# Performance work log

Hardware: AMD Instinct MI355X
Metric: run time of the kernel (lower is better)

Reference implementation:

```python
import jax, jax.numpy as jnp
import numpy as np

H = 2048

def setup_inputs() -> dict:
    key = jax.random.key(0)
    ks = jax.random.split(key, 7)
    s = 1.0 / np.sqrt(H)
    return {
        "input": jax.random.normal(ks[0], (2, 4096, H), dtype=jnp.float32),
        "Wq": jax.random.uniform(ks[1], (H, H), jnp.float32, -s, s),
        "bq": jax.random.uniform(ks[2], (H,), jnp.float32, -s, s),
        "Wk": jax.random.uniform(ks[3], (H, H), jnp.float32, -s, s),
        "bk": jax.random.uniform(ks[4], (H,), jnp.float32, -s, s),
        "Wv": jax.random.uniform(ks[5], (H, H), jnp.float32, -s, s),
        "bv": jax.random.uniform(ks[6], (H,), jnp.float32, -s, s),
    }

def reference(input, Wq, bq, Wk, bk, Wv, bv):
    # Linear projections: y = x @ W^T + b (torch nn.Linear convention)
    q = jnp.einsum('bsh,oh->bso', input, Wq) + bq
    k = jnp.einsum('bsh,oh->bso', input, Wk) + bk
    v = jnp.einsum('bsh,oh->bso', input, Wv) + bv
    # NOTE: original module has NO 1/sqrt(d) scaling and NO mask
    scores = jnp.einsum('bqh,bkh->bqk', q, k)          # [B,S,S]
    attn = jax.nn.softmax(scores, axis=-1)
    out = jnp.einsum('bqk,bkh->bqh', attn, v)           # [B,S,H]
    return out
```

## Files before the change

kernel.cpp:

```cpp
#include <hip/hip_runtime.h>
#include <hip/hip_bf16.h>
#include <cstdint>
#include <cstddef>


typedef _Float16 half8 __attribute__((ext_vector_type(8)));
typedef _Float16 half4 __attribute__((ext_vector_type(4)));
typedef float    f32x4 __attribute__((ext_vector_type(4)));

__device__ __forceinline__ void gld_lds16(const void* g, void* l) {
  __builtin_amdgcn_global_load_lds(
      (const __attribute__((address_space(1))) unsigned int*)g,
      (__attribute__((address_space(3))) unsigned int*)l, 16, 0, 0);
}

#define FENCE()  asm volatile("" ::: "memory")
#define VMC(n)   asm volatile("s_waitcnt vmcnt(" #n ")" ::: "memory")
#define SBARF()  do { __builtin_amdgcn_s_barrier(); FENCE(); } while (0)
#define PRIO1()  __builtin_amdgcn_s_setprio(1)
#define PRIO0()  __builtin_amdgcn_s_setprio(0)

#define LOAD_A(dst, RB, MH) do {                                            \
  const char* _p = ldsA + ((RB)*2 + wr) * 16384 + fr * 128;                 \
  _Pragma("unroll") for (int mi = 0; mi < 4; ++mi) {                        \
    dst[mi][0] = *(const half8*)(_p + ((MH)*4 + mi) * 2048 + cS0);          \
    dst[mi][1] = *(const half8*)(_p + ((MH)*4 + mi) * 2048 + cS1);          \
  }                                                                         \
} while (0)

#define LOAD_B(dst, RB, NH) do {                                            \
  const char* _p = ldsB + ((RB)*2 + (wc >> 1)) * 16384 +                    \
                   ((wc & 1) * 64 + fr) * 128;                              \
  _Pragma("unroll") for (int ni = 0; ni < 2; ++ni) {                        \
    dst[ni][0] = *(const half8*)(_p + ((NH)*2 + ni) * 2048 + cS0);          \
    dst[ni][1] = *(const half8*)(_p + ((NH)*2 + ni) * 2048 + cS1);          \
  }                                                                         \
} while (0)

#define MFMA_Q(AF, BF, MH, NH)                                              \
  _Pragma("unroll") for (int mi = 0; mi < 4; ++mi)                          \
  _Pragma("unroll") for (int ni = 0; ni < 2; ++ni) {                        \
    f32x4& _c = acc[(MH)*4 + mi][(NH)*2 + ni];                              \
    _c = __builtin_amdgcn_mfma_f32_16x16x32_f16(AF[mi][0], BF[ni][0], _c, 0, 0, 0); \
    _c = __builtin_amdgcn_mfma_f32_16x16x32_f16(AF[mi][1], BF[ni][1], _c, 0, 0, 0); \
  }

#define STAGE8(BSEL, KO) do {                                               \
  const size_t _k = (KO);                                                   \
  gld_lds16(Asrc + _k,               ldsc + (BSEL)*32768 + wvd);            \
  gld_lds16(Asrc + _k + lda8,        ldsc + (BSEL)*32768 + wvd + 1024);     \
  gld_lds16(Asrc + _k + ldaH,        ldsc + (BSEL)*32768 + 16384 + wvd);    \
  gld_lds16(Asrc + _k + ldaH + lda8, ldsc + (BSEL)*32768 + 16384 + wvd + 1024); \
  gld_lds16(Bsrc + _k,               ldsc + 65536 + (BSEL)*32768 + wvd);    \
  gld_lds16(Bsrc + _k + ldb8,        ldsc + 65536 + (BSEL)*32768 + wvd + 1024); \
  gld_lds16(Bsrc + _k + ldbH,        ldsc + 65536 + (BSEL)*32768 + 16384 + wvd); \
  gld_lds16(Bsrc + _k + ldbH + ldb8, ldsc + 65536 + (BSEL)*32768 + 16384 + wvd + 1024); \
} while (0)

#define TILEB(RB, KO, DO_STAGE) do {                                        \
  LOAD_A(af0, RB, 0);                                                       \
  LOAD_B(b0,  RB, 0);                                                       \
  if (DO_STAGE) STAGE8((RB)^1, KO);                                         \
  LOAD_B(b1,  RB, 1);                                                       \
  LOAD_A(af1, RB, 1);                                                       \
  PRIO1();                                                                  \
  MFMA_Q(af0, b0, 0, 0);                                                    \
  MFMA_Q(af0, b1, 0, 1);                                                    \
  MFMA_Q(af1, b1, 1, 1);                                                    \
  MFMA_Q(af1, b0, 1, 0);                                                    \
  PRIO0();                                                                  \
  VMC(0);                                                                   \
  SBARF();                                                                  \
} while (0)

template <int MODE>
__global__ __launch_bounds__(512, 2) void gemm256(
    const _Float16* __restrict__ A, int lda,
    const _Float16* __restrict__ B, int ldb,
    const float* __restrict__ bias,
    void* __restrict__ out, int ldo, int K,
    size_t sA, size_t sB, size_t sO)
{
  __shared__ __attribute__((aligned(128))) char lds[131072];
  char* ldsc = (char*)lds;
  char* ldsA = ldsc;
  char* ldsB = ldsc + 65536;

  const int tid  = threadIdx.x;
  const int wv   = tid >> 6;
  const int lane = tid & 63;
  const int wr = wv >> 2;
  const int wc = wv & 3;
  const int bm = blockIdx.x * 256;
  const int bn = blockIdx.y * 256;
  A += (size_t)blockIdx.z * sA;
  B += (size_t)blockIdx.z * sB;

  const int fr = lane & 15;
  const int kq = lane >> 4;
  const int sx = (fr & 7) << 4;
  const int cS0 = (kq * 16) ^ sx;
  const int cS1 = (64 + kq * 16) ^ sx;
  const int lr  = lane >> 3;
  const int sc8 = ((lane & 7) ^ (lr & 7)) << 3;

  const _Float16* Asrc = A + (size_t)(bm + wv * 16 + lr) * lda + sc8;
  const _Float16* Bsrc = B + (size_t)(bn + wv * 16 + lr) * ldb + sc8;
  const size_t lda8 = (size_t)lda * 8,  ldaH = (size_t)lda * 128;
  const size_t ldb8 = (size_t)ldb * 8,  ldbH = (size_t)ldb * 128;
  const int wvd = wv * 2048;

  f32x4 acc[8][4];
  const f32x4 zf = {0.f, 0.f, 0.f, 0.f};
#pragma unroll
  for (int mi = 0; mi < 8; ++mi)
#pragma unroll
    for (int ni = 0; ni < 4; ++ni) acc[mi][ni] = zf;

  half8 af0[4][2], af1[4][2], b0[2][2], b1[2][2];

  const int NT = K >> 6;
  const int NI = NT >> 1;

  STAGE8(0, 0);
  VMC(0);
  SBARF();

  for (int it = 0; it < NI; ++it) {
    const size_t kA = (size_t)(2 * it + 1) * 64;
    const size_t kB = (size_t)(2 * it + 2) * 64;
    const bool sB = (2 * it + 2) < NT;
    TILEB(0, kA, 1);
    TILEB(1, kB, sB);
  }

#pragma unroll
  for (int mi = 0; mi < 8; ++mi) {
#pragma unroll
    for (int ni = 0; ni < 4; ++ni) {
      const int col  = bn + wc * 64 + ni * 16 + fr;
      const int row0 = bm + wr * 128 + mi * 16 + kq * 4;
      const f32x4 a = acc[mi][ni];
      if constexpr (MODE == 0) {
        float* O = (float*)out + (size_t)blockIdx.z * sO;
#pragma unroll
        for (int j = 0; j < 4; ++j) O[(size_t)(row0 + j) * ldo + col] = a[j];
      } else if constexpr (MODE == 1) {
        _Float16* O = (_Float16*)out;
        const float bb = bias[col];
#pragma unroll
        for (int j = 0; j < 4; ++j)
          O[(size_t)(row0 + j) * ldo + col] = (_Float16)(a[j] + bb);
      } else {
        _Float16* O = (_Float16*)out;
        const float bb = bias[col];
        half4 h;
#pragma unroll
        for (int j = 0; j < 4; ++j) h[j] = (_Float16)(a[j] + bb);
        *(half4*)(O + (size_t)col * ldo + row0) = h;
      }
    }
  }
}

__device__ __forceinline__ float wave_max_f(float v) {
#pragma unroll
  for (int o = 32; o; o >>= 1) v = fmaxf(v, __shfl_xor(v, o));
  return v;
}
__device__ __forceinline__ float wave_sum_f(float v) {
#pragma unroll
  for (int o = 32; o; o >>= 1) v += __shfl_xor(v, o);
  return v;
}

__global__ __launch_bounds__(256) void softmax_rows(
    const float* __restrict__ S, _Float16* __restrict__ P)
{
  __shared__ float rmax[4], rsum[4];
  const int tid = threadIdx.x;
  const float* s = S + (size_t)blockIdx.x * 4096;
  _Float16*    p = P + (size_t)blockIdx.x * 4096;

  f32x4 v[4];
  float m = -3.0e38f;
#pragma unroll
  for (int i = 0; i < 4; ++i) {
    v[i] = ((const f32x4*)s)[i * 256 + tid];
#pragma unroll
    for (int j = 0; j < 4; ++j) m = fmaxf(m, v[i][j]);
  }
  m = wave_max_f(m);
  if ((tid & 63) == 0) rmax[tid >> 6] = m;
  __syncthreads();
  m = fmaxf(fmaxf(rmax[0], rmax[1]), fmaxf(rmax[2], rmax[3]));

  float e[16];
  float sum = 0.f;
#pragma unroll
  for (int i = 0; i < 4; ++i)
#pragma unroll
    for (int j = 0; j < 4; ++j) {
      const float t = __expf(v[i][j] - m);
      e[i * 4 + j] = t;
      sum += t;
    }
  sum = wave_sum_f(sum);
  if ((tid & 63) == 0) rsum[tid >> 6] = sum;
  __syncthreads();
  sum = rsum[0] + rsum[1] + rsum[2] + rsum[3];
  const float inv = 1.0f / sum;

#pragma unroll
  for (int i = 0; i < 4; ++i) {
    half4 h;
#pragma unroll
    for (int j = 0; j < 4; ++j) h[j] = (_Float16)(e[i * 4 + j] * inv);
    ((half4*)p)[i * 256 + tid] = h;
  }
}

__global__ __launch_bounds__(256) void cvt_f32_f16(
    const float* __restrict__ in, _Float16* __restrict__ out, int n4)
{
  const int stride = gridDim.x * 256;
  for (int idx = blockIdx.x * 256 + threadIdx.x; idx < n4; idx += stride) {
    const f32x4 x = ((const f32x4*)in)[idx];
    half4 h;
#pragma unroll
    for (int j = 0; j < 4; ++j) h[j] = (_Float16)x[j];
    ((half4*)out)[idx] = h;
  }
}

extern "C" void kernel_launch(void* const* d_in, const int* in_sizes, int n_in,
                              void* d_out, int out_size, void* d_ws, size_t ws_size,
                              hipStream_t stream)
{
  const float* X  = (const float*)d_in[0];
  const float* Wq = (const float*)d_in[1];
  const float* bq = (const float*)d_in[2];
  const float* Wk = (const float*)d_in[3];
  const float* bk = (const float*)d_in[4];
  const float* Wv = (const float*)d_in[5];
  const float* bv = (const float*)d_in[6];
  float* out = (float*)d_out;

  const size_t NX = (size_t)2 * 4096 * 2048;
  const size_t NW = (size_t)2048 * 2048;
  const size_t NS = (size_t)2 * 4096 * 4096;

  char* w = (char*)d_ws;
  float*    Ssc = (float*)w;
  _Float16* Xh  = (_Float16*)w;
  _Float16* Wqh = (_Float16*)(w + NX * 2);
  _Float16* Wkh = (_Float16*)(w + NX * 2 + NW * 2);
  _Float16* Wvh = (_Float16*)(w + NX * 2 + 2 * NW * 2);
  _Float16* Q   = (_Float16*)(w + NS * 4);
  _Float16* Kp  = (_Float16*)(w + NS * 4 + NX * 2);
  _Float16* P   = (_Float16*)(w + NS * 4);
  _Float16* Vt  = (_Float16*)(w + NS * 4 + 2 * NX * 2);

  cvt_f32_f16<<<2048, 256, 0, stream>>>(X,  Xh,  (int)(NX / 4));
  cvt_f32_f16<<<512,  256, 0, stream>>>(Wq, Wqh, (int)(NW / 4));
  cvt_f32_f16<<<512,  256, 0, stream>>>(Wk, Wkh, (int)(NW / 4));
  cvt_f32_f16<<<512,  256, 0, stream>>>(Wv, Wvh, (int)(NW / 4));

  const dim3 blk(512);
  gemm256<1><<<dim3(32, 8, 1), blk, 0, stream>>>(Xh, 2048, Wqh, 2048, bq,
                                                 Q, 2048, 2048, 0, 0, 0);
  gemm256<1><<<dim3(32, 8, 1), blk, 0, stream>>>(Xh, 2048, Wkh, 2048, bk,
                                                 Kp, 2048, 2048, 0, 0, 0);
  gemm256<2><<<dim3(32, 8, 1), blk, 0, stream>>>(Xh, 2048, Wvh, 2048, bv,
                                                 Vt, 8192, 2048, 0, 0, 0);
  gemm256<0><<<dim3(16, 16, 2), blk, 0, stream>>>(
      Q, 2048, Kp, 2048, nullptr, Ssc, 4096, 2048,
      (size_t)4096 * 2048, (size_t)4096 * 2048, (size_t)4096 * 4096);
  softmax_rows<<<8192, 256, 0, stream>>>(Ssc, P);
  gemm256<0><<<dim3(16, 8, 2), blk, 0, stream>>>(
      P, 4096, Vt, 8192, nullptr, out, 2048, 4096,
      (size_t)4096 * 4096, (size_t)4096, (size_t)4096 * 2048);
}
```

Measured before the change: 548.4 us.

## Restructure GEMM main loop into eight-phase ping-pong schedule with split staging

Replaces the two-tile-per-iteration GEMM loop with an eight-phase schedule. Each phase interleaves one LDS fragment read, one half of a global-to-LDS stage, and one MFMA quadrant, separated by barriers and lgkm/vm waits. B tiles are prefetched further ahead and wait counts are relaxed so global loads can overlap several compute phases. It also drops the min-blocks-per-CU launch bound, which frees register allocation at possible occupancy cost, and reuses one A fragment buffer to cut registers. The extra barriers and waits add synchronisation overhead.

```diff
diff --git a/kernel.cpp b/kernel.cpp
--- a/kernel.cpp
+++ b/kernel.cpp
@@ -15,8 +15,10 @@
 }
 
 #define FENCE()  asm volatile("" ::: "memory")
+#define LGKM(n)  asm volatile("s_waitcnt lgkmcnt(" #n ")" ::: "memory")
 #define VMC(n)   asm volatile("s_waitcnt vmcnt(" #n ")" ::: "memory")
-#define SBARF()  do { __builtin_amdgcn_s_barrier(); FENCE(); } while (0)
+#define SBAR()   do { __builtin_amdgcn_s_barrier(); FENCE(); } while (0)
+#define SCHED0() __builtin_amdgcn_sched_barrier(0)
 #define PRIO1()  __builtin_amdgcn_s_setprio(1)
 #define PRIO0()  __builtin_amdgcn_s_setprio(0)
 
@@ -45,36 +47,23 @@
     _c = __builtin_amdgcn_mfma_f32_16x16x32_f16(AF[mi][1], BF[ni][1], _c, 0, 0, 0); \
   }
 
-#define STAGE8(BSEL, KO) do {                                               \
-  const size_t _k = (KO);                                                   \
-  gld_lds16(Asrc + _k,               ldsc + (BSEL)*32768 + wvd);            \
-  gld_lds16(Asrc + _k + lda8,        ldsc + (BSEL)*32768 + wvd + 1024);     \
-  gld_lds16(Asrc + _k + ldaH,        ldsc + (BSEL)*32768 + 16384 + wvd);    \
-  gld_lds16(Asrc + _k + ldaH + lda8, ldsc + (BSEL)*32768 + 16384 + wvd + 1024); \
-  gld_lds16(Bsrc + _k,               ldsc + 65536 + (BSEL)*32768 + wvd);    \
-  gld_lds16(Bsrc + _k + ldb8,        ldsc + 65536 + (BSEL)*32768 + wvd + 1024); \
-  gld_lds16(Bsrc + _k + ldbH,        ldsc + 65536 + (BSEL)*32768 + 16384 + wvd); \
-  gld_lds16(Bsrc + _k + ldbH + ldb8, ldsc + 65536 + (BSEL)*32768 + 16384 + wvd + 1024); \
-} while (0)
-
-#define TILEB(RB, KO, DO_STAGE) do {                                        \
-  LOAD_A(af0, RB, 0);                                                       \
-  LOAD_B(b0,  RB, 0);                                                       \
-  if (DO_STAGE) STAGE8((RB)^1, KO);                                         \
-  LOAD_B(b1,  RB, 1);                                                       \
-  LOAD_A(af1, RB, 1);                                                       \
-  PRIO1();                                                                  \
-  MFMA_Q(af0, b0, 0, 0);                                                    \
-  MFMA_Q(af0, b1, 0, 1);                                                    \
-  MFMA_Q(af1, b1, 1, 1);                                                    \
-  MFMA_Q(af1, b0, 1, 0);                                                    \
-  PRIO0();                                                                  \
-  VMC(0);                                                                   \
-  SBARF();                                                                  \
-} while (0)
+#define STAGE_A(bsel, h, kof)                                               \
+  {                                                                         \
+    const _Float16* _s = Abase + (size_t)((h) * 128) * lda + (kof);         \
+    char* _d = ldsA + ((bsel)*2 + (h)) * 16384 + wvd;                       \
+    gld_lds16(_s, _d);                                                      \
+    gld_lds16(_s + lda8, _d + 1024);                                        \
+  }
+#define STAGE_B(bsel, h, kof)                                               \
+  {                                                                         \
+    const _Float16* _s = Bbase + (size_t)((h) * 128) * ldb + (kof);         \
+    char* _d = ldsB + ((bsel)*2 + (h)) * 16384 + wvd;                       \
+    gld_lds16(_s, _d);                                                      \
+    gld_lds16(_s + ldb8, _d + 1024);                                        \
+  }
 
 template <int MODE>
-__global__ __launch_bounds__(512, 2) void gemm256(
+__global__ __launch_bounds__(512) void gemm256(
     const _Float16* __restrict__ A, int lda,
     const _Float16* __restrict__ B, int ldb,
     const float* __restrict__ bias,
@@ -82,9 +71,8 @@
     size_t sA, size_t sB, size_t sO)
 {
   __shared__ __attribute__((aligned(128))) char lds[131072];
-  char* ldsc = (char*)lds;
-  char* ldsA = ldsc;
-  char* ldsB = ldsc + 65536;
+  char* ldsA = (char*)lds;
+  char* ldsB = (char*)lds + 65536;
 
   const int tid  = threadIdx.x;
   const int wv   = tid >> 6;
@@ -104,10 +92,9 @@
   const int lr  = lane >> 3;
   const int sc8 = ((lane & 7) ^ (lr & 7)) << 3;
 
-  const _Float16* Asrc = A + (size_t)(bm + wv * 16 + lr) * lda + sc8;
-  const _Float16* Bsrc = B + (size_t)(bn + wv * 16 + lr) * ldb + sc8;
-  const size_t lda8 = (size_t)lda * 8,  ldaH = (size_t)lda * 128;
-  const size_t ldb8 = (size_t)ldb * 8,  ldbH = (size_t)ldb * 128;
+  const _Float16* Abase = A + (size_t)(bm + wv * 16 + lr) * lda + sc8;
+  const _Float16* Bbase = B + (size_t)(bn + wv * 16 + lr) * ldb + sc8;
+  const size_t lda8 = (size_t)lda * 8, ldb8 = (size_t)ldb * 8;
   const int wvd = wv * 2048;
 
   f32x4 acc[8][4];
@@ -117,21 +104,65 @@
 #pragma unroll
     for (int ni = 0; ni < 4; ++ni) acc[mi][ni] = zf;
 
-  half8 af0[4][2], af1[4][2], b0[2][2], b1[2][2];
+  half8 af[4][2], bf0[2][2], bf1[2][2];
 
   const int NT = K >> 6;
   const int NI = NT >> 1;
 
-  STAGE8(0, 0);
-  VMC(0);
-  SBARF();
+  STAGE_A(0, 0, 0); STAGE_A(0, 1, 0); STAGE_B(0, 0, 0); STAGE_B(0, 1, 0);
+  STAGE_B(1, 0, 64); STAGE_B(1, 1, 64);
+  VMC(4);
+  SBAR();
 
   for (int it = 0; it < NI; ++it) {
-    const size_t kA = (size_t)(2 * it + 1) * 64;
-    const size_t kB = (size_t)(2 * it + 2) * 64;
-    const bool sB = (2 * it + 2) < NT;
-    TILEB(0, kA, 1);
-    TILEB(1, kB, sB);
+    const bool more = (it < NI - 1);
+    const size_t t1k = (size_t)(2 * it + 1) * 64;
+    const size_t t2k = t1k + 64;
+    const size_t t3k = t1k + 128;
+
+    LOAD_A(af, 0, 0); LOAD_B(bf0, 0, 0);
+    STAGE_A(1, 0, t1k);
+    LGKM(8);
+    SBAR(); LGKM(0); SCHED0();
+    PRIO1(); MFMA_Q(af, bf0, 0, 0); PRIO0();
+    SBAR();
+    LOAD_B(bf1, 0, 1);
+    STAGE_A(1, 1, t1k);
+    SBAR(); LGKM(0); SCHED0();
+    PRIO1(); MFMA_Q(af, bf1, 0, 1); PRIO0();
+    SBAR();
+    LOAD_A(af, 0, 1);
+    if (more) STAGE_B(0, 0, t2k);
+    SBAR(); LGKM(0); SCHED0();
+    PRIO1(); MFMA_Q(af, bf1, 1, 1); PRIO0();
+    SBAR();
+    if (more) STAGE_B(0, 1, t2k);
+    SBAR(); SCHED0();
+    PRIO1(); MFMA_Q(af, bf0, 1, 0); PRIO0();
+    if (more) { VMC(4); } else { VMC(0); }
+    SBAR();
+
+    LOAD_A(af, 1, 0); LOAD_B(bf0, 1, 0);
+    if (more) STAGE_A(0, 0, t2k);
+    LGKM(8);
+    SBAR(); LGKM(0); SCHED0();
+    PRIO1(); MFMA_Q(af, bf0, 0, 0); PRIO0();
+    SBAR();
+    LOAD_B(bf1, 1, 1);
+    if (more) STAGE_A(0, 1, t2k);
+    SBAR(); LGKM(0); SCHED0();
+    PRIO1(); MFMA_Q(af, bf1, 0, 1); PRIO0();
+    SBAR();
+    LOAD_A(af, 1, 1);
+    if (more) STAGE_B(1, 0, t3k);
+    SBAR(); LGKM(0); SCHED0();
+    PRIO1(); MFMA_Q(af, bf1, 1, 1); PRIO0();
+    SBAR();
+    if (more) STAGE_B(1, 1, t3k);
+    SBAR(); SCHED0();
+    PRIO1(); MFMA_Q(af, bf0, 1, 0); PRIO0();
+    if (more) { VMC(4); } else { VMC(0); }
+    SBAR();
   }
 
 #pragma unroll
```

Measured after the change: 494.3 us. 9.9% less time.
